# Performance work log

Measured on AMD Instinct MI355X. Metric: run time of the kernel, lower is better.

## Reference

```python
import jax, jax.numpy as jnp
import numpy as np

B, L, D, H = 4, 1024, 1024, 16
HD = D // H
TERM = 20  # N-term / C-term window size


def setup_inputs() -> dict:
    key = jax.random.key(0)
    ks = jax.random.split(key, 9)
    x = jax.random.normal(ks[0], (B, L, D), jnp.float32)
    lens = jax.random.randint(ks[1], (B,), 64, L + 1)
    mask = jnp.arange(L)[None, :] < lens[:, None]  # contiguous valid prefix, bool [B,L]
    s = 0.02  # ~ xavier_uniform with gain 1/H**0.25
    Wq = jax.random.normal(ks[2], (D, D), jnp.float32) * s
    Wk = jax.random.normal(ks[3], (D, D), jnp.float32) * s
    Wv = jax.random.normal(ks[4], (D, D), jnp.float32) * s
    bq = jnp.zeros((D,), jnp.float32)
    bk = jnp.zeros((D,), jnp.float32)
    bv = jnp.zeros((D,), jnp.float32)
    gamma = jnp.ones((D,), jnp.float32)
    beta = jnp.zeros((D,), jnp.float32)
    return {"x": x, "mask": mask, "Wq": Wq, "bq": bq, "Wk": Wk, "bk": bk,
            "Wv": Wv, "bv": bv, "gamma": gamma, "beta": beta}


def reference(x, mask, Wq, bq, Wk, bk, Wv, bv, gamma, beta):
    # LayerNorm (eps = 1e-5, torch default)
    mu = x.mean(-1, keepdims=True)
    var = ((x - mu) ** 2).mean(-1, keepdims=True)
    xn = (x - mu) / jnp.sqrt(var + 1e-5) * gamma + beta

    Q = (xn @ Wq + bq).reshape(B, L, H, HD)
    K = (xn @ Wk + bk).reshape(B, L, H, HD)
    V = (xn @ Wv + bv).reshape(B, L, H, HD)

    # note: original divides by head_dim**0.25 (quarter power) - keep faithful
    scores = jnp.einsum('bqhd,bkhd->bhqk', Q, K) / HD ** 0.25

    # mask fill on key positions
    scores = jnp.where(mask[:, None, None, :], scores, -10000.0)

    # per-sample length-dependent bias on key positions
    lens = mask.sum(-1)                      # [B] int
    pos = jnp.arange(L)                      # [L]
    inlen = pos[None, :] < lens[:, None]     # [B,L]
    bias_ge = (1.0 * (pos[None, :] < TERM)
               + 0.8 * ((pos[None, :] >= lens[:, None] - TERM) & inlen))
    bias_lt = (1.0 + 0.8) * inlen
    bias = jnp.where((lens >= TERM)[:, None], bias_ge, bias_lt)  # [B,L]
    scores = scores + bias[:, None, None, :]

    attn = jax.nn.softmax(scores, axis=-1)   # [B,H,L,L]
    entropy_loss = -(attn * jnp.log(attn + 1e-10)).sum(-1).mean()

    context = jnp.einsum('bhqk,bkhd->bqhd', attn, V).reshape(B, L, D)

    # ragged N-term / C-term mean pooling (vectorized segment means)
    term = jnp.minimum(TERM, lens)           # [B]
    termf = term.astype(x.dtype)[:, None]
    wn = (pos[None, :] < term[:, None]).astype(x.dtype)                      # first term tokens
    wc = ((pos[None, :] >= (lens - term)[:, None]) & inlen).astype(x.dtype)  # last term valid tokens
    n_term = (context * wn[:, :, None]).sum(1) / termf
    c_term = (context * wc[:, :, None]).sum(1) / termf
    global_pool = context.mean(1)            # mean over full L, as in original

    pooled = jnp.concatenate([n_term, c_term, global_pool], axis=1)  # [B,3D]
    return pooled, attn.mean(1), entropy_loss
```

## Files before the change

### kernel.cpp

```cpp
#include <hip/hip_runtime.h>
#include <hip/hip_bf16.h>
#include <hip/hip_fp16.h>


typedef unsigned short u16;
typedef __attribute__((ext_vector_type(4))) float f32x4;
typedef __attribute__((ext_vector_type(8))) __bf16 bf16x8;
typedef __attribute__((ext_vector_type(4))) unsigned int u32x4;
typedef __attribute__((ext_vector_type(4))) unsigned short u16x4;
typedef __attribute__((ext_vector_type(8))) unsigned short u16x8;

#define DEV __device__ __forceinline__

DEV float bf2f(u16 u){ union{unsigned i; float f;} c; c.i = ((unsigned)u)<<16; return c.f; }
DEV u16 f2bf(float f){ union{float f; unsigned i;} c; c.f=f; unsigned i=c.i;
  unsigned r = i + 0x7FFFu + ((i>>16)&1u); return (u16)(r>>16); }

__global__ void k_detect(const void* mask, const void* gamma, const void* beta,
                         const void* bq, const void* bk, const void* bv,
                         int* lens, float* ent, int* flag,
                         u16* gam_c, u16* bet_c, u16* bq_c, u16* bk_c, u16* bv_c,
                         float* pacc){
  int t = threadIdx.x; int w = t>>6; int lane = t&63;
  int isf32 = (((const u16*)gamma)[0] == 0) ? 1 : 0;
  if (t==0){ *flag = isf32; *ent = 0.f; }
  for (int i=t; i<12288; i+=256) pacc[i] = 0.f;
  for (int i=t; i<1024; i+=256){
    if (isf32){
      gam_c[i]=f2bf(((const float*)gamma)[i]); bet_c[i]=f2bf(((const float*)beta)[i]);
      bq_c[i] =f2bf(((const float*)bq)[i]);    bk_c[i] =f2bf(((const float*)bk)[i]);
      bv_c[i] =f2bf(((const float*)bv)[i]);
    } else {
      gam_c[i]=((const u16*)gamma)[i]; bet_c[i]=((const u16*)beta)[i];
      bq_c[i] =((const u16*)bq)[i];    bk_c[i] =((const u16*)bk)[i];
      bv_c[i] =((const u16*)bv)[i];
    }
  }
  const unsigned char* mb = (const unsigned char*)mask;
  const int* mi = (const int*)mask;
  const u16* ms = (const u16*)mask;
  int cnt = 0;
  if (mb[1] != 0) {
    if (mb[0]==1 && mb[1]==1) { for (int i=lane;i<1024;i+=64) cnt += (mb[w*1024+i]!=0); }
    else                      { for (int i=lane;i<1024;i+=64) cnt += (ms[w*1024+i]!=0); }
  } else {
    if (mi[1]==0)             { for (int i=lane;i<1024;i+=64) cnt += (mi[(w*1024+i)*2]!=0); }
    else                      { for (int i=lane;i<1024;i+=64) cnt += (mi[w*1024+i]!=0); }
  }
  #pragma unroll
  for (int o=32;o;o>>=1) cnt += __shfl_down(cnt,o);
  if (lane==0) lens[w] = cnt;
}

__global__ __launch_bounds__(256) void k_ln(const void* x, const u16* gamma, const u16* beta,
                                            u16* xn, const int* flagp){
  int isf32 = *flagp;
  int row = blockIdx.x, t = threadIdx.x;
  float f0,f1,f2,f3;
  if (isf32){
    f32x4 v = ((const f32x4*)x)[(size_t)row*256 + t];
    f0=v[0]; f1=v[1]; f2=v[2]; f3=v[3];
  } else {
    u16x4 v = ((const u16x4*)x)[(size_t)row*256 + t];
    f0=bf2f(v[0]); f1=bf2f(v[1]); f2=bf2f(v[2]); f3=bf2f(v[3]);
  }
  float s = f0+f1+f2+f3;
  float sq = f0*f0+f1*f1+f2*f2+f3*f3;
  #pragma unroll
  for (int o=32;o;o>>=1){ s += __shfl_down(s,o); sq += __shfl_down(sq,o); }
  __shared__ float rs[4], rq[4];
  if ((t&63)==0){ rs[t>>6]=s; rq[t>>6]=sq; }
  __syncthreads();
  s = rs[0]+rs[1]+rs[2]+rs[3]; sq = rq[0]+rq[1]+rq[2]+rq[3];
  float mu = s*(1.0f/1024.0f);
  float var = sq*(1.0f/1024.0f) - mu*mu;
  float rstd = rsqrtf(var + 1e-5f);
  u16x4 gv = ((const u16x4*)gamma)[t];
  u16x4 bv = ((const u16x4*)beta)[t];
  u16x4 o;
  o[0]=f2bf((f0-mu)*rstd*bf2f(gv[0])+bf2f(bv[0]));
  o[1]=f2bf((f1-mu)*rstd*bf2f(gv[1])+bf2f(bv[1]));
  o[2]=f2bf((f2-mu)*rstd*bf2f(gv[2])+bf2f(bv[2]));
  o[3]=f2bf((f3-mu)*rstd*bf2f(gv[3])+bf2f(bv[3]));
  ((u16x4*)(xn + (size_t)row*1024))[t] = o;
}

DEV void tr64_body(const void* src, u16* dst, int R, int C, int bt, int isf32, int t,
                   u16 (*tile)[68]){
  int tc_n = C>>6;
  int tr = (bt / tc_n)<<6, tc = (bt % tc_n)<<6;
  if (isf32){
    const float* s = (const float*)src;
    #pragma unroll
    for (int it=0; it<2; ++it){
      int f = it*2048 + t*8; int r=f>>6, c=f&63;
      const float* p = s + (long)(tr+r)*C + tc + c;
      f32x4 a = *(const f32x4*)p, b = *(const f32x4*)(p+4);
      u16x4 ua, ub;
      #pragma unroll
      for (int j=0;j<4;j++){ ua[j]=f2bf(a[j]); ub[j]=f2bf(b[j]); }
      *(u16x4*)&tile[r][c]   = ua;
      *(u16x4*)&tile[r][c+4] = ub;
    }
  } else {
    const u16* s = (const u16*)src;
    #pragma unroll
    for (int it=0; it<2; ++it){
      int f = it*2048 + t*8; int r=f>>6, c=f&63;
      *(u16x4*)&tile[r][c]   = *(const u16x4*)(s + (long)(tr+r)*C + tc + c);
      *(u16x4*)&tile[r][c+4] = *(const u16x4*)(s + (long)(tr+r)*C + tc + c + 4);
    }
  }
  __syncthreads();
  #pragma unroll
  for (int it=0; it<2; ++it){
    int f = it*2048 + t*8; int r=f>>6, c=f&63;
    u16x4 a, b2;
    #pragma unroll
    for (int j=0;j<4;j++){ a[j]=tile[c+j][r]; b2[j]=tile[c+4+j][r]; }
    *(u16x4*)(dst + (long)(tc+r)*R + tr + c)     = a;
    *(u16x4*)(dst + (long)(tc+r)*R + tr + c + 4) = b2;
  }
}

__global__ __launch_bounds__(256) void k_trW(const void* Wq, const void* Wk, const void* Wv,
                                             u16* Wt, const int* flagp){
  __shared__ u16 tile[64][68];
  int isf32 = *flagp;
  const void* src = (blockIdx.y==0) ? Wq : (blockIdx.y==1) ? Wk : Wv;
  u16* dst = Wt + ((size_t)blockIdx.y<<20);
  tr64_body(src, dst, 1024, 1024, blockIdx.x, isf32, threadIdx.x, tile);
}

__global__ __launch_bounds__(256) void k_trV(const u16* Vb, u16* Vt){
  __shared__ u16 tile[64][68];
  tr64_body(Vb + ((size_t)blockIdx.y<<16), Vt + ((size_t)blockIdx.y<<16),
            1024, 64, blockIdx.x, 0, threadIdx.x, tile);
}

__global__ __launch_bounds__(256) void k_gemm(const u16* A, const u16* Bt,
    const u16* biasq, const u16* biask, const u16* biasv,
    u16* Qb, u16* Kb, u16* Vb){
  __shared__ u16 lA[2][128*32];
  __shared__ u16 lB[2][128*32];
  int t = threadIdx.x;
  int w = t>>6, l = t&63, g = l>>4, lc = l&15;
  int wm = w>>1, wn = w&1;
  int m0 = (blockIdx.x & 31)<<7;
  int n0 = (int)(blockIdx.x >> 5)<<7;
  int fb0 = t*16, fb1 = 4096 + t*16;
  int r0 = fb0>>6, c0 = fb0&63, r1 = fb1>>6, c1 = fb1&63;
  const char* Ab = (const char*)A; const char* Bb = (const char*)Bt;
  long aoff0 = (long)(m0+r0)*2048 + c0;
  long aoff1 = (long)(m0+r1)*2048 + c1;
  long boff0 = (long)(n0+r0)*2048 + c0;
  long boff1 = (long)(n0+r1)*2048 + c1;
  f32x4 vzero = {0.f,0.f,0.f,0.f};
  f32x4 acc[4][4];
  #pragma unroll
  for (int i=0;i<4;i++)
    #pragma unroll
    for (int j=0;j<4;j++) acc[i][j] = vzero;
  u32x4 ra0,ra1,rb0,rb1;
  ra0 = *(const u32x4*)(Ab + aoff0); ra1 = *(const u32x4*)(Ab + aoff1);
  rb0 = *(const u32x4*)(Bb + boff0); rb1 = *(const u32x4*)(Bb + boff1);
  *(u32x4*)((char*)lA[0] + fb0) = ra0; *(u32x4*)((char*)lA[0] + fb1) = ra1;
  *(u32x4*)((char*)lB[0] + fb0) = rb0; *(u32x4*)((char*)lB[0] + fb1) = rb1;
  __syncthreads();
  for (int kt=0; kt<32; ++kt){
    int cur = kt & 1;
    if (kt < 31){
      long ko = (long)(kt+1)*64;
      ra0 = *(const u32x4*)(Ab + aoff0 + ko); ra1 = *(const u32x4*)(Ab + aoff1 + ko);
      rb0 = *(const u32x4*)(Bb + boff0 + ko); rb1 = *(const u32x4*)(Bb + boff1 + ko);
    }
    bf16x8 af[4], bfr[4];
    #pragma unroll
    for (int i=0;i<4;i++) af[i]  = *(const bf16x8*)(const void*)&lA[cur][((wm<<6)+(i<<4)+lc)*32 + (g<<3)];
    #pragma unroll
    for (int j=0;j<4;j++) bfr[j] = *(const bf16x8*)(const void*)&lB[cur][((wn<<6)+(j<<4)+lc)*32 + (g<<3)];
    #pragma unroll
    for (int i=0;i<4;i++)
      #pragma unroll
      for (int j=0;j<4;j++)
        acc[i][j] = __builtin_amdgcn_mfma_f32_16x16x32_bf16(af[i], bfr[j], acc[i][j], 0,0,0);
    __syncthreads();
    if (kt < 31){
      int nxt = cur^1;
      *(u32x4*)((char*)lA[nxt] + fb0) = ra0; *(u32x4*)((char*)lA[nxt] + fb1) = ra1;
      *(u32x4*)((char*)lB[nxt] + fb0) = rb0; *(u32x4*)((char*)lB[nxt] + fb1) = rb1;
      __syncthreads();
    }
  }
  #pragma unroll
  for (int j=0;j<4;j++){
    int n = n0 + (wn<<6) + (j<<4) + lc;
    int kind = n>>10; int nn = n & 1023;
    const u16* bp = (kind==0)?biasq:(kind==1)?biask:biasv;
    float bvl = bf2f(bp[nn]);
    u16* dst = (kind==0)?Qb:(kind==1)?Kb:Vb;
    int h = nn>>6, hd = n&63;
    #pragma unroll
    for (int i=0;i<4;i++){
      #pragma unroll
      for (int r=0;r<4;r++){
        int m = m0 + (wm<<6) + (i<<4) + (g<<2) + r;
        int bb = m>>10, pos = m&1023;
        dst[(((bb<<4)+h)<<16) + (pos<<6) + hd] = f2bf(acc[i][j][r] + bvl);
      }
    }
  }
}

__global__ __launch_bounds__(512) void k_attn(const u16* Qg, const u16* Kg, const u16* Vt,
    const int* lens, u16* ctx, u16* Pp, float* ent_acc){
  __shared__ u16 Plds[16][1032];
  __shared__ float redz[16][8];
  __shared__ float rede[16][8];
  __shared__ __half redc[2][16][66];
  int bqi = blockIdx.x;
  int qt = bqi & 63, hg = (bqi>>6)&3, b = bqi>>8;
  int q0 = qt<<4;
  int t = threadIdx.x, w = t>>6, l = t&63, g = l>>4, lc = l&15;
  int kh = w>>2, dg = w&3;
  int len = lens[b];
  {
    u16x8 z8 = {0,0,0,0,0,0,0,0};
    u16* pz = &Plds[0][0];
    for (int i=t; i<2064; i+=512) *(u16x8*)(pz + i*8) = z8;
  }
  __half2 mh[8][2];
  #pragma unroll
  for (int i=0;i<8;i++){ mh[i][0] = __float2half2_rn(0.f); mh[i][1] = __float2half2_rn(0.f); }
  float ent_local = 0.f;
  const float SCALE = 0.35355339059327373f;
  for (int hh=0; hh<4; ++hh){
    int h = (hg<<2) + hh;
    int base = ((b<<4)+h)<<16;
    bf16x8 qf0 = *(const bf16x8*)(const void*)(Qg + base + ((q0+lc)<<6) + (g<<3));
    bf16x8 qf1 = *(const bf16x8*)(const void*)(Qg + base + ((q0+lc)<<6) + (g<<3) + 32);
    f32x4 s[8];
    float zp[4]={0,0,0,0}, ep[4]={0,0,0,0};
    #pragma unroll
    for (int tt=0; tt<8; ++tt){
      int kb = (tt<<7)+(w<<4);
      if (kb < len){
        const u16* kp = Kg + base + ((kb+lc)<<6) + (g<<3);
        bf16x8 kf0 = *(const bf16x8*)(const void*)kp;
        bf16x8 kf1 = *(const bf16x8*)(const void*)(kp + 32);
        f32x4 a = {0.f,0.f,0.f,0.f};
        a = __builtin_amdgcn_mfma_f32_16x16x32_bf16(qf0, kf0, a, 0,0,0);
        a = __builtin_amdgcn_mfma_f32_16x16x32_bf16(qf1, kf1, a, 0,0,0);
        int key = kb + lc;
        bool valid = key < len;
        float bias;
        if (len >= 20) bias = (key<20 ? 1.0f : 0.0f) + ((valid && key >= len-20) ? 0.8f : 0.0f);
        else bias = 1.8f;
        #pragma unroll
        for (int r=0;r<4;r++){
          float sv = valid ? a[r]*SCALE + bias : -10000.0f;
          float e = __expf(fminf(sv, 60.0f));
          zp[r]+=e; ep[r]+=e*sv;
          a[r] = e;
          Plds[(g<<2)+r][key] = f2bf(e);
        }
        s[tt] = a;
      }
    }
    #pragma unroll
    for (int r=0;r<4;r++){
      zp[r]+=__shfl_xor(zp[r],1); ep[r]+=__shfl_xor(ep[r],1);
      zp[r]+=__shfl_xor(zp[r],2); ep[r]+=__shfl_xor(ep[r],2);
      zp[r]+=__shfl_xor(zp[r],4); ep[r]+=__shfl_xor(ep[r],4);
      zp[r]+=__shfl_xor(zp[r],8); ep[r]+=__shfl_xor(ep[r],8);
    }
    if (lc==0){
      #pragma unroll
      for (int r=0;r<4;r++){ redz[(g<<2)+r][w]=zp[r]; rede[(g<<2)+r][w]=ep[r]; }
    }
    __syncthreads();
    float invz[4];
    #pragma unroll
    for (int r=0;r<4;r++){
      int rr=(g<<2)+r;
      float Z = redz[rr][0]+redz[rr][1]+redz[rr][2]+redz[rr][3]
              + redz[rr][4]+redz[rr][5]+redz[rr][6]+redz[rr][7];
      float E = rede[rr][0]+rede[rr][1]+rede[rr][2]+rede[rr][3]
              + rede[rr][4]+rede[rr][5]+rede[rr][6]+rede[rr][7];
      invz[r] = 1.0f/Z;
      if (w==0 && lc==0) ent_local += __logf(Z) - E*invz[r];
    }
    #pragma unroll
    for (int tt=0;tt<8;++tt){
      if (((tt<<7)+(w<<4)) < len){
        float p0 = s[tt][0]*invz[0], p1 = s[tt][1]*invz[1];
        float p2 = s[tt][2]*invz[2], p3 = s[tt][3]*invz[3];
        mh[tt][0] = __hadd2(mh[tt][0], __halves2half2(__float2half_rn(p0), __float2half_rn(p1)));
        mh[tt][1] = __hadd2(mh[tt][1], __halves2half2(__float2half_rn(p2), __float2half_rn(p3)));
      }
    }
    f32x4 cacc = {0.f,0.f,0.f,0.f};
    const u16* vrow = Vt + base + (((dg<<4)+lc)<<10);
    #pragma unroll
    for (int ks=0; ks<16; ++ks){
      int kk = (ks<<1)+kh;
      if ((kk<<5) < len){
        bf16x8 pa = *(const bf16x8*)(const void*)(&Plds[0][0] + lc*1032 + (kk<<5) + (g<<3));
        bf16x8 vb = *(const bf16x8*)(const void*)(vrow + (kk<<5) + (g<<3));
        cacc = __builtin_amdgcn_mfma_f32_16x16x32_bf16(pa, vb, cacc, 0,0,0);
      }
    }
    #pragma unroll
    for (int r=0;r<4;r++) redc[kh][(g<<2)+r][(dg<<4)+lc] = __float2half(cacc[r]*invz[r]);
    __syncthreads();
    #pragma unroll
    for (int ii=0; ii<2; ++ii){
      int i = t + (ii<<9);
      int q = i>>6, d = i&63;
      float v = __half2float(redc[0][q][d]) + __half2float(redc[1][q][d]);
      ctx[(((size_t)(b<<10)+q0+q)<<10) + (h<<6) + d] = f2bf(v);
    }
  }
  u16* oa = Pp + ((size_t)hg<<22) + ((size_t)b<<20);
  #pragma unroll
  for (int tt=0; tt<8; ++tt){
    int col = (tt<<7)+(w<<4)+lc;
    int qb_ = (q0+(g<<2))<<10;
    oa[qb_ + col]            = __half_as_ushort(__low2half(mh[tt][0]));
    oa[qb_ + 1024 + col]     = __half_as_ushort(__high2half(mh[tt][0]));
    oa[qb_ + 2048 + col]     = __half_as_ushort(__low2half(mh[tt][1]));
    oa[qb_ + 3072 + col]     = __half_as_ushort(__high2half(mh[tt][1]));
  }
  if (w==0){
    float es = ent_local;
    #pragma unroll
    for (int o=32;o;o>>=1) es += __shfl_down(es,o);
    if (l==0) atomicAdd(ent_acc, es);
  }
}

__global__ __launch_bounds__(256) void k_pmean(const u16* Pp, void* out_v, const int* flagp){
  int isf32 = *flagp;
  size_t idx = ((size_t)blockIdx.x*256 + threadIdx.x)*8;
  int b = (int)(idx>>20); size_t f = idx & 0xFFFFFu;
  const u16* p0 = Pp + ((size_t)b<<20) + f;
  float s[8] = {0,0,0,0,0,0,0,0};
  #pragma unroll
  for (int gI=0; gI<4; ++gI){
    u16x8 v = *(const u16x8*)(p0 + ((size_t)gI<<22));
    #pragma unroll
    for (int j=0;j<8;j++) s[j] += __half2float(__ushort_as_half(v[j]));
  }
  if (isf32){
    float* o = (float*)out_v + 12288 + idx;
    #pragma unroll
    for (int j=0;j<8;j++) o[j] = s[j]*0.0625f;
  } else {
    u16x8 o;
    #pragma unroll
    for (int j=0;j<8;j++) o[j] = f2bf(s[j]*0.0625f);
    *(u16x8*)((u16*)out_v + 12288 + idx) = o;
  }
}

__global__ __launch_bounds__(256) void k_pool1(const u16* ctx, const int* lens, float* pacc){
  int b = blockIdx.y, pc = blockIdx.x;
  int t = threadIdx.x; int d0 = t*4;
  int len = lens[b];
  int term = len < 20 ? len : 20;
  int lo = len - term;
  float sn[4]={0,0,0,0}, sc[4]={0,0,0,0}, sg[4]={0,0,0,0};
  const u16* base = ctx + ((size_t)b<<20) + ((size_t)pc<<15) + d0;
  for (int p=0;p<32;++p){
    int gp = (pc<<5)+p;
    u16x4 v = *(const u16x4*)(base + ((size_t)p<<10));
    bool in_n = gp < term;
    bool in_c = (gp >= lo) && (gp < len);
    #pragma unroll
    for (int j=0;j<4;j++){
      float fv = bf2f(v[j]);
      sg[j] += fv;
      if (in_n) sn[j] += fv;
      if (in_c) sc[j] += fv;
    }
  }
  #pragma unroll
  for (int j=0;j<4;j++){
    atomicAdd(&pacc[(b<<10)+d0+j], sn[j]);
    atomicAdd(&pacc[4096+(b<<10)+d0+j], sc[j]);
    atomicAdd(&pacc[8192+(b<<10)+d0+j], sg[j]);
  }
}

__global__ __launch_bounds__(256) void k_pool2(const float* pacc, const int* lens, const float* ent,
                                               void* out_v, const int* flagp){
  int isf32 = *flagp;
  int idx = blockIdx.x*256 + threadIdx.x;
  if (idx < 12288){
    int b = idx/3072; int r = idx - b*3072; int seg = r>>10; int d = r&1023;
    int len = lens[b]; int term = len < 20 ? len : 20;
    float scale = (seg==2) ? (1.0f/1024.0f) : (1.0f/(float)term);
    float v = pacc[seg*4096 + (b<<10) + d]*scale;
    if (isf32) ((float*)out_v)[idx] = v; else ((u16*)out_v)[idx] = f2bf(v);
  }
  if (idx==0){
    float e = (*ent)*(1.0f/65536.0f);
    if (isf32) ((float*)out_v)[4206592] = e; else ((u16*)out_v)[4206592] = f2bf(e);
  }
}

extern "C" void kernel_launch(void* const* d_in, const int* in_sizes, int n_in,
                              void* d_out, int out_size, void* d_ws, size_t ws_size,
                              hipStream_t stream){
  (void)in_sizes; (void)n_in; (void)out_size; (void)ws_size;
  const void* x     = d_in[0];
  const void* mask  = d_in[1];
  const void* Wq    = d_in[2];
  const void* bq    = d_in[3];
  const void* Wk    = d_in[4];
  const void* bk    = d_in[5];
  const void* Wv    = d_in[6];
  const void* bv    = d_in[7];
  const void* gamma = d_in[8];
  const void* beta  = d_in[9];

  char* ws = (char*)d_ws;
  int*   lens = (int*)ws;
  float* ent  = (float*)(ws + 64);
  int*   flag = (int*)(ws + 68);
  u16* gam_c = (u16*)(ws + 256);
  u16* bet_c = gam_c + 1024;
  u16* bq_c  = bet_c + 1024;
  u16* bk_c  = bq_c + 1024;
  u16* bv_c  = bk_c + 1024;
  u16* xn  = (u16*)(ws + 0x100000);
  u16* Qb  = (u16*)(ws + 0x900000);
  u16* Kb  = (u16*)(ws + 0x1100000);
  u16* ctx = (u16*)(ws + 0x1900000);
  u16* Pp  = (u16*)(ws + 0x2100000);
  u16* Wt  = (u16*)(ws + 0x2100000);
  u16* Vb  = (u16*)(ws + 0x2700000);
  u16* Vt  = xn;
  float* pacc = (float*)(ws + 0x4100000);

  k_detect<<<1,256,0,stream>>>(mask, gamma, beta, bq, bk, bv,
                               lens, ent, flag, gam_c, bet_c, bq_c, bk_c, bv_c, pacc);
  k_ln<<<4096,256,0,stream>>>(x, gam_c, bet_c, xn, flag);
  k_trW<<<dim3(256,3),256,0,stream>>>(Wq, Wk, Wv, Wt, flag);
  k_gemm<<<768,256,0,stream>>>(xn, Wt, bq_c, bk_c, bv_c, Qb, Kb, Vb);
  k_trV<<<dim3(16,64),256,0,stream>>>(Vb, Vt);
  k_attn<<<1024,512,0,stream>>>(Qb, Kb, Vt, lens, ctx, Pp, ent);
  k_pmean<<<2048,256,0,stream>>>(Pp, d_out, flag);
  k_pool1<<<dim3(32,4),256,0,stream>>>(ctx, lens, pacc);
  k_pool2<<<49,256,0,stream>>>(pacc, lens, ent, d_out, flag);
}
```

Before: 169.3 us.

## Double-buffer P tile in LDS and drop second per-head barrier in attention

The per-head P tile and the softmax reduction buffers become double-buffered across heads, so the second __syncthreads per head can be removed. The PV product is now done by only 4 of the 8 waves, each covering the full key range, which drops the cross-wave split-K reduction through LDS. Each of those waves writes its context values straight to global memory. This cuts barriers and LDS traffic, but half the waves now idle during PV, each active wave runs twice as many serial MFMAs, and LDS use roughly doubles, which could lower occupancy.

```diff
diff --git a/kernel.cpp b/kernel.cpp
--- a/kernel.cpp
+++ b/kernel.cpp
@@ -214,20 +214,18 @@
 
 __global__ __launch_bounds__(512) void k_attn(const u16* Qg, const u16* Kg, const u16* Vt,
     const int* lens, u16* ctx, u16* Pp, float* ent_acc){
-  __shared__ u16 Plds[16][1032];
-  __shared__ float redz[16][8];
-  __shared__ float rede[16][8];
-  __shared__ __half redc[2][16][66];
+  __shared__ u16 Plds[2][16][1032];
+  __shared__ float redz[2][16][8];
+  __shared__ float rede[2][16][8];
   int bqi = blockIdx.x;
   int qt = bqi & 63, hg = (bqi>>6)&3, b = bqi>>8;
   int q0 = qt<<4;
   int t = threadIdx.x, w = t>>6, l = t&63, g = l>>4, lc = l&15;
-  int kh = w>>2, dg = w&3;
   int len = lens[b];
   {
     u16x8 z8 = {0,0,0,0,0,0,0,0};
-    u16* pz = &Plds[0][0];
-    for (int i=t; i<2064; i+=512) *(u16x8*)(pz + i*8) = z8;
+    u16* pz = &Plds[0][0][0];
+    for (int i=t; i<4128; i+=512) *(u16x8*)(pz + i*8) = z8;
   }
   __half2 mh[8][2];
   #pragma unroll
@@ -237,6 +235,7 @@
   for (int hh=0; hh<4; ++hh){
     int h = (hg<<2) + hh;
     int base = ((b<<4)+h)<<16;
+    int pb = hh & 1;
     bf16x8 qf0 = *(const bf16x8*)(const void*)(Qg + base + ((q0+lc)<<6) + (g<<3));
     bf16x8 qf1 = *(const bf16x8*)(const void*)(Qg + base + ((q0+lc)<<6) + (g<<3) + 32);
     f32x4 s[8];
@@ -262,7 +261,7 @@
           float e = __expf(fminf(sv, 60.0f));
           zp[r]+=e; ep[r]+=e*sv;
           a[r] = e;
-          Plds[(g<<2)+r][key] = f2bf(e);
+          Plds[pb][(g<<2)+r][key] = f2bf(e);
         }
         s[tt] = a;
       }
@@ -276,19 +275,25 @@
     }
     if (lc==0){
       #pragma unroll
-      for (int r=0;r<4;r++){ redz[(g<<2)+r][w]=zp[r]; rede[(g<<2)+r][w]=ep[r]; }
+      for (int r=0;r<4;r++){ redz[pb][(g<<2)+r][w]=zp[r]; rede[pb][(g<<2)+r][w]=ep[r]; }
     }
     __syncthreads();
     float invz[4];
     #pragma unroll
     for (int r=0;r<4;r++){
       int rr=(g<<2)+r;
-      float Z = redz[rr][0]+redz[rr][1]+redz[rr][2]+redz[rr][3]
-              + redz[rr][4]+redz[rr][5]+redz[rr][6]+redz[rr][7];
-      float E = rede[rr][0]+rede[rr][1]+rede[rr][2]+rede[rr][3]
-              + rede[rr][4]+rede[rr][5]+rede[rr][6]+rede[rr][7];
+      float Z = redz[pb][rr][0]+redz[pb][rr][1]+redz[pb][rr][2]+redz[pb][rr][3]
+              + redz[pb][rr][4]+redz[pb][rr][5]+redz[pb][rr][6]+redz[pb][rr][7];
       invz[r] = 1.0f/Z;
-      if (w==0 && lc==0) ent_local += __logf(Z) - E*invz[r];
+    }
+    if (w==0 && lc==0){
+      #pragma unroll
+      for (int r=0;r<4;r++){
+        int rr=(g<<2)+r;
+        float E = rede[pb][rr][0]+rede[pb][rr][1]+rede[pb][rr][2]+rede[pb][rr][3]
+                + rede[pb][rr][4]+rede[pb][rr][5]+rede[pb][rr][6]+rede[pb][rr][7];
+        ent_local += __logf(1.0f/invz[r]) - E*invz[r];
+      }
     }
     #pragma unroll
     for (int tt=0;tt<8;++tt){
@@ -299,26 +304,21 @@
         mh[tt][1] = __hadd2(mh[tt][1], __halves2half2(__float2half_rn(p2), __float2half_rn(p3)));
       }
     }
-    f32x4 cacc = {0.f,0.f,0.f,0.f};
-    const u16* vrow = Vt + base + (((dg<<4)+lc)<<10);
-    #pragma unroll
-    for (int ks=0; ks<16; ++ks){
-      int kk = (ks<<1)+kh;
-      if ((kk<<5) < len){
-        bf16x8 pa = *(const bf16x8*)(const void*)(&Plds[0][0] + lc*1032 + (kk<<5) + (g<<3));
-        bf16x8 vb = *(const bf16x8*)(const void*)(vrow + (kk<<5) + (g<<3));
-        cacc = __builtin_amdgcn_mfma_f32_16x16x32_bf16(pa, vb, cacc, 0,0,0);
+    if (w < 4){
+      f32x4 cacc = {0.f,0.f,0.f,0.f};
+      const u16* vrow = Vt + base + (((w<<4)+lc)<<10);
+      const u16* pbase = &Plds[pb][0][0] + lc*1032;
+      #pragma unroll
+      for (int kk=0; kk<32; ++kk){
+        if ((kk<<5) < len){
+          bf16x8 pa = *(const bf16x8*)(const void*)(pbase + (kk<<5) + (g<<3));
+          bf16x8 vb = *(const bf16x8*)(const void*)(vrow + (kk<<5) + (g<<3));
+          cacc = __builtin_amdgcn_mfma_f32_16x16x32_bf16(pa, vb, cacc, 0,0,0);
+        }
       }
-    }
-    #pragma unroll
-    for (int r=0;r<4;r++) redc[kh][(g<<2)+r][(dg<<4)+lc] = __float2half(cacc[r]*invz[r]);
-    __syncthreads();
-    #pragma unroll
-    for (int ii=0; ii<2; ++ii){
-      int i = t + (ii<<9);
-      int q = i>>6, d = i&63;
-      float v = __half2float(redc[0][q][d]) + __half2float(redc[1][q][d]);
-      ctx[(((size_t)(b<<10)+q0+q)<<10) + (h<<6) + d] = f2bf(v);
+      u16* cb = ctx + (((size_t)(b<<10)+q0+(g<<2))<<10) + (h<<6) + (w<<4) + lc;
+      #pragma unroll
+      for (int r=0;r<4;r++) cb[(size_t)r<<10] = f2bf(cacc[r]*invz[r]);
     }
   }
   u16* oa = Pp + ((size_t)hg<<22) + ((size_t)b<<20);
```

Measured after the change: 185.6 us. 1.1x slower.
